# Kernel optimization log

Hardware: AMD Instinct MI355X
Metric: run time of the kernel (lower is better)

Reference implementation:

```python
import jax, jax.numpy as jnp
import numpy as np

N_GRAPHS = 256
EPS = 1e-5


def _bn(x, g, b):
    # training-mode BatchNorm1d: biased batch statistics
    m = jnp.mean(x, axis=0)
    v = jnp.mean((x - m) ** 2, axis=0)
    return (x - m) * jax.lax.rsqrt(v + EPS) * g + b


def _gcn_conv(x, W, b, src, dst, dinv, n_nodes):
    # GCNConv: D^{-1/2} (A + I) D^{-1/2} X W + b
    h = x @ W  # [N, H]
    coef = dinv[src] * dinv[dst]  # [E]
    msg = h[src] * coef[:, None]  # [E, H]
    agg = jax.ops.segment_sum(msg, dst, num_segments=n_nodes)
    agg = agg + h * (dinv * dinv)[:, None]  # self-loop term
    return agg + b


def setup_inputs() -> dict:
    key = jax.random.key(0)
    ks = jax.random.split(key, 20)
    N, E, D, H, C = 50000, 600000, 128, 128, 10
    L = 3  # num_conv_layers
    x = jax.random.normal(ks[0], (N, D), dtype=jnp.float32)
    edge_index = jax.random.randint(ks[1], (2, E), 0, N, dtype=jnp.int64)
    batch = jnp.sort(jax.random.randint(ks[2], (N,), 0, N_GRAPHS, dtype=jnp.int64))

    def xavier(k, shape):
        fan_in, fan_out = shape[0], shape[1]
        lim = float(np.sqrt(6.0 / (fan_in + fan_out)))
        return jax.random.uniform(k, shape, jnp.float32, -lim, lim)

    return {
        "x": x,
        "edge_index": edge_index,
        "batch": batch,
        "bn_feat_g": jnp.ones((D,), jnp.float32),
        "bn_feat_b": jnp.full((D,), 1e-4, jnp.float32),
        "conv_feat_W": xavier(ks[3], (D, H)),
        "conv_feat_b": jnp.zeros((H,), jnp.float32),
        "conv_W": jnp.stack([xavier(ks[4 + i], (H, H)) for i in range(L)]),
        "conv_b": jnp.zeros((L, H), jnp.float32),
        "bn_conv_g": jnp.ones((L, H), jnp.float32),
        "bn_conv_b": jnp.full((L, H), 1e-4, jnp.float32),
        "gate_W1": xavier(ks[8], (H, H)),
        "gate_b1": jnp.zeros((H,), jnp.float32),
        "gate_W2": xavier(ks[9], (H, 1)),
        "gate_b2": jnp.zeros((1,), jnp.float32),
        "fc_W": xavier(ks[10], (H, H)),
        "fc_b": jnp.zeros((H,), jnp.float32),
        "bn_fc_g": jnp.ones((H,), jnp.float32),
        "bn_fc_b": jnp.full((H,), 1e-4, jnp.float32),
        "cls_W": xavier(ks[11], (H, C)),
        "cls_b": jnp.zeros((C,), jnp.float32),
    }


def reference(x, edge_index, batch, bn_feat_g, bn_feat_b, conv_feat_W, conv_feat_b,
              conv_W, conv_b, bn_conv_g, bn_conv_b, gate_W1, gate_b1, gate_W2,
              gate_b2, fc_W, fc_b, bn_fc_g, bn_fc_b, cls_W, cls_b):
    N = x.shape[0]
    src, dst = edge_index[0], edge_index[1]
    # degree incl. self-loop (edge weights = 1)
    deg = jax.ops.segment_sum(jnp.ones_like(src, dtype=x.dtype), dst, num_segments=N) + 1.0
    dinv = jax.lax.rsqrt(deg)

    h = _bn(x, bn_feat_g, bn_feat_b)
    h = jax.nn.relu(_gcn_conv(h, conv_feat_W, conv_feat_b, src, dst, dinv, N))
    for i in range(conv_W.shape[0]):
        h = jax.nn.relu(_gcn_conv(_bn(h, bn_conv_g[i], bn_conv_b[i]),
                                  conv_W[i], conv_b[i], src, dst, dinv, N))
    gate = jax.nn.sigmoid(jax.nn.relu(h @ gate_W1 + gate_b1) @ gate_W2 + gate_b2)  # [N,1]
    g = jax.ops.segment_sum(h * gate, batch, num_segments=N_GRAPHS)  # [G, H]
    g = jax.nn.relu(_bn(g, bn_fc_g, bn_fc_b) @ fc_W + fc_b)
    logits = g @ cls_W + cls_b
    return jax.nn.log_softmax(logits, axis=-1)
```

## Files before the change

kernel.cpp:

```cpp
#include <hip/hip_runtime.h>
#include <hip/hip_fp16.h>

typedef unsigned short u16;
typedef unsigned int u32;
typedef __attribute__((ext_vector_type(8))) short short8;
typedef __attribute__((ext_vector_type(4))) float floatx4;

#define EPSI 1e-5f
#define NCOPY 64

__device__ __forceinline__ float b2f(u16 h) { return __uint_as_float(((u32)h) << 16); }
__device__ __forceinline__ u16 f2b(float f) {
    u32 u = __float_as_uint(f);
    return (u16)((u + 0x7fffu + ((u >> 16) & 1u)) >> 16);
}
__device__ __forceinline__ u32 pack2(float a, float b) {
    return (u32)f2b(a) | ((u32)f2b(b) << 16);
}
__device__ __forceinline__ float ldf(const void* p, int i, int fm) {
    if (fm == 1) return b2f(((const u16*)p)[i]);
    if (fm == 2) return __half2float(__ushort_as_half(((const u16*)p)[i]));
    return ((const float*)p)[i];
}
__device__ __forceinline__ int ldi(const void* p, int i, int im) {
    return im ? ((const int*)p)[2 * i] : ((const int*)p)[i];
}

template <typename T>
__device__ __forceinline__ void ntst(T* p, T v) {
    __builtin_nontemporal_store(v, p);
}

__device__ __forceinline__ void acc8(float* a, int4 v, float w) {
    u32 x = (u32)v.x, y = (u32)v.y, z = (u32)v.z, q = (u32)v.w;
    a[0] += b2f((u16)x) * w;
    a[1] += b2f((u16)(x >> 16)) * w;
    a[2] += b2f((u16)y) * w;
    a[3] += b2f((u16)(y >> 16)) * w;
    a[4] += b2f((u16)z) * w;
    a[5] += b2f((u16)(z >> 16)) * w;
    a[6] += b2f((u16)q) * w;
    a[7] += b2f((u16)(q >> 16)) * w;
}

__global__ void init_kernel(u32* zp, int nz, const void* ones, const void* ei, int* flags) {
    int i = blockIdx.x * 256 + threadIdx.x;
    if (i < nz) zp[i] = 0;
    if (blockIdx.x == 0 && threadIdx.x == 0) {
        u32 w = ((const u32*)ones)[0];
        int fm = 0;
        if (w == 0x3F803F80u) fm = 1;
        else if (w == 0x3C003C00u) fm = 2;
        const u32* e = (const u32*)ei;
        int all0 = 1;
        for (int k = 0; k < 16; ++k)
            if (e[2 * k + 1] != 0u) all0 = 0;
        flags[0] = fm;
        flags[1] = all0;
    }
}

__global__ void bigprep_kernel(const void* __restrict__ ei, int* __restrict__ cnt, int E,
                               const void* __restrict__ batch, int* __restrict__ bounds, int N,
                               int EB, const void* __restrict__ x, u32* __restrict__ A2,
                               float* __restrict__ stats0, const void* __restrict__ gW1,
                               const void* __restrict__ gb1, u16* __restrict__ Wtg,
                               float* __restrict__ bias2g, const void* __restrict__ cfW,
                               const void* __restrict__ cW, u16* __restrict__ Wt4,
                               const void* __restrict__ fcW, float* __restrict__ fcWf,
                               const void* __restrict__ clsW, float* __restrict__ clsWf,
                               const void* __restrict__ fcb, float* __restrict__ fcbf,
                               const void* __restrict__ clsb, float* __restrict__ clsbf,
                               const void* __restrict__ gW2, float* __restrict__ gW2f,
                               const void* __restrict__ gb2, float* __restrict__ gb2f,
                               const void* __restrict__ cfb, const void* __restrict__ cvb,
                               float* __restrict__ biasf, u16* __restrict__ rank,
                               const int* __restrict__ flags) {
    int fm = flags[0];
    int bid = blockIdx.x, t = threadIdx.x;
    if (bid < EB) {
        int im = flags[1];
        int g = bid * 256 + t;
        if (g < E) {
            int r = atomicAdd(&cnt[ldi(ei, E + g, im)], 1);
            rank[g] = (u16)r;
        }
        if (g < N) {
            int b = ldi(batch, g, im);
            if (g == 0) {
                for (int q = 0; q <= b; ++q) bounds[q] = 0;
            } else {
                int bp = ldi(batch, g - 1, im);
                for (int q = bp + 1; q <= b; ++q) bounds[q] = g;
            }
            if (g == N - 1) {
                for (int q = b + 1; q <= 256; ++q) bounds[q] = N;
            }
        }
        return;
    }
    int pid = bid - EB;
    if (pid < 1024) {
        int np = N * 64;
        float s0 = 0.f, s1 = 0.f, q0 = 0.f, q1 = 0.f;
        if (fm == 1) {
            const u32* xs = (const u32*)x;
            for (int j = pid * 256 + t; j < np; j += 1024 * 256) {
                u32 w = xs[j];
                ntst(&A2[j], w);
                float v0 = b2f((u16)w), v1 = b2f((u16)(w >> 16));
                s0 += v0;
                q0 += v0 * v0;
                s1 += v1;
                q1 += v1 * v1;
            }
        } else if (fm == 0) {
            const float2* xs2 = (const float2*)x;
            for (int j = pid * 256 + t; j < np; j += 1024 * 256) {
                float2 v = xs2[j];
                ntst(&A2[j], pack2(v.x, v.y));
                s0 += v.x;
                q0 += v.x * v.x;
                s1 += v.y;
                q1 += v.y * v.y;
            }
        } else {
            for (int j = pid * 256 + t; j < np; j += 1024 * 256) {
                float v0 = ldf(x, 2 * j, fm);
                float v1 = ldf(x, 2 * j + 1, fm);
                ntst(&A2[j], pack2(v0, v1));
                s0 += v0;
                q0 += v0 * v0;
                s1 += v1;
                q1 += v1 * v1;
            }
        }
        __shared__ float2 sh[256];
        sh[t] = make_float2(s0, s1);
        __syncthreads();
        float* so = stats0 + (pid & (NCOPY - 1)) * 256;
        if (t < 64) {
            float a = 0.f, b = 0.f;
#pragma unroll
            for (int w = 0; w < 4; ++w) {
                float2 v = sh[t + w * 64];
                a += v.x;
                b += v.y;
            }
            atomicAdd(&so[2 * t], a);
            atomicAdd(&so[2 * t + 1], b);
        }
        __syncthreads();
        sh[t] = make_float2(q0, q1);
        __syncthreads();
        if (t < 64) {
            float a = 0.f, b = 0.f;
#pragma unroll
            for (int w = 0; w < 4; ++w) {
                float2 v = sh[t + w * 64];
                a += v.x;
                b += v.y;
            }
            atomicAdd(&so[128 + 2 * t], a);
            atomicAdd(&so[128 + 2 * t + 1], b);
        }
    } else if (pid < 1152) {
        int n = pid - 1024;
        if (t < 128) Wtg[n * 128 + t] = f2b(ldf(gW1, t * 128 + n, fm));
        if (t == 0) bias2g[n] = ldf(gb1, n, fm);
    } else if (pid < 1216) {
        int task = pid - 1152;
        int mat = task >> 4, tile = task & 15;
        int tr = (tile >> 2) * 32, tc = (tile & 3) * 32;
        const void* src = mat == 0 ? cfW : cW;
        int soff = mat == 0 ? 0 : (mat - 1) * 16384;
        __shared__ float tb[32][33];
#pragma unroll
        for (int i = 0; i < 4; ++i) {
            int o = t * 4 + i;
            int r = o >> 5, c = o & 31;
            tb[r][c] = ldf(src, soff + (tr + r) * 128 + tc + c, fm);
        }
        __syncthreads();
        u16* dst = Wt4 + mat * 16384;
#pragma unroll
        for (int i = 0; i < 4; ++i) {
            int o = t * 4 + i;
            int nr = o >> 5, kc = o & 31;
            dst[(tc + nr) * 128 + tr + kc] = f2b(tb[kc][nr]);
        }
    } else if (pid < 1224) {
        int base = (pid - 1216) * 2048;
        for (int i = t; i < 2048; i += 256) fcWf[base + i] = ldf(fcW, base + i, fm);
    } else {
        for (int i = t; i < 1280; i += 256) clsWf[i] = ldf(clsW, i, fm);
        for (int i = t; i < 512; i += 256)
            biasf[i] = (i < 128) ? ldf(cfb, i, fm) : ldf(cvb, i - 128, fm);
        if (t < 128) {
            fcbf[t] = ldf(fcb, t, fm);
            gW2f[t] = ldf(gW2, t, fm);
        }
        if (t < 10) clsbf[t] = ldf(clsb, t, fm);
        if (t == 0) gb2f[0] = ldf(gb2, 0, fm);
    }
}

__global__ void scan_kernel(const int* __restrict__ cnt, int* __restrict__ row_start, int n) {
    int b = blockIdx.x, t = threadIdx.x;
    __shared__ int sh[256];
    const int4* c4 = (const int4*)cnt;
    int lim4 = b * 256;
    int acc = 0;
    for (int i = t; i < lim4; i += 256) {
        int4 v = c4[i];
        acc += v.x + v.y + v.z + v.w;
    }
    sh[t] = acc;
    __syncthreads();
    for (int o = 128; o > 0; o >>= 1) {
        if (t < o) sh[t] += sh[t + o];
        __syncthreads();
    }
    int pre = sh[0];
    __syncthreads();
    int base = b * 1024 + t * 4;
    int v[4];
    int s = 0;
#pragma unroll
    for (int j = 0; j < 4; ++j) {
        int idx = base + j;
        v[j] = (idx < n) ? cnt[idx] : 0;
        s += v[j];
    }
    sh[t] = s;
    __syncthreads();
    for (int o = 1; o < 256; o <<= 1) {
        int add = (t >= o) ? sh[t - o] : 0;
        __syncthreads();
        sh[t] += add;
        __syncthreads();
    }
    int run = pre + sh[t] - s;
#pragma unroll
    for (int j = 0; j < 4; ++j) {
        int idx = base + j;
        run += v[j];
        if (idx < n) row_start[idx + 1] = run;
    }
    if (b == 0 && t == 0) row_start[0] = 0;
}

__global__ __launch_bounds__(256) void mfma_fill_kernel(
    const u16* __restrict__ A, const u16* __restrict__ Wt, const float* __restrict__ stats,
    const void* __restrict__ bng, const void* __restrict__ bnb, u16* __restrict__ C, int N,
    int mmgrid, const void* __restrict__ ei, const int* __restrict__ row_start,
    const u16* __restrict__ rank, const int* __restrict__ cnt, u32* __restrict__ edges, int E,
    const int* __restrict__ flags) {
    int t = threadIdx.x;
    if ((int)blockIdx.x >= mmgrid) {
        int im = flags[1];
        int e = (blockIdx.x - mmgrid) * 256 + t;
        if (e < E) {
            int s = ldi(ei, e, im);
            int d = ldi(ei, E + e, im);
            int p = row_start[d] + (int)rank[e];
            float ds = rsqrtf((float)cnt[s] + 1.0f);
            edges[p] = (u32)s | ((u32)__half_as_ushort(__float2half_rn(ds)) << 16);
        }
        return;
    }
    int fm = flags[0];
    __shared__ float scs[128], shs[128];
    if (t < 128) {
        float ms = 0.f, qs = 0.f;
#pragma unroll
        for (int c = 0; c < NCOPY; ++c) {
            ms += stats[c * 256 + t];
            qs += stats[c * 256 + 128 + t];
        }
        float m = ms / (float)N;
        float var = qs / (float)N - m * m;
        float rs = rsqrtf(var + EPSI);
        float sc = rs * ldf(bng, t, fm);
        scs[t] = sc;
        shs[t] = ldf(bnb, t, fm) - m * sc;
    }
    __syncthreads();
    int wid = t >> 6, lane = t & 63;
    int m16 = lane & 15, q = lane >> 4;
    int row0 = blockIdx.x * 64 + wid * 16;
    if (row0 >= N) return;
    int arow = row0 + m16;
    floatx4 acc[8];
#pragma unroll
    for (int i = 0; i < 8; ++i) acc[i] = (floatx4){0.f, 0.f, 0.f, 0.f};
#pragma unroll
    for (int kc = 0; kc < 4; ++kc) {
        short8 af;
        if (arow < N) {
            short8 raw = *(const short8*)&A[(size_t)arow * 128 + kc * 32 + q * 8];
            int k0 = kc * 32 + q * 8;
#pragma unroll
            for (int j = 0; j < 8; ++j)
                af[j] = (short)f2b(b2f((u16)raw[j]) * scs[k0 + j] + shs[k0 + j]);
        } else {
#pragma unroll
            for (int j = 0; j < 8; ++j) af[j] = 0;
        }
#pragma unroll
        for (int nt = 0; nt < 8; ++nt) {
            short8 bf = *(const short8*)&Wt[(nt * 16 + m16) * 128 + kc * 32 + q * 8];
            acc[nt] = __builtin_amdgcn_mfma_f32_16x16x32_bf16(af, bf, acc[nt], 0, 0, 0);
        }
    }
#pragma unroll
    for (int nt = 0; nt < 8; ++nt) {
#pragma unroll
        for (int reg = 0; reg < 4; ++reg) {
            int r = row0 + q * 4 + reg;
            if (r < N) C[(size_t)r * 128 + nt * 16 + m16] = f2b(acc[nt][reg]);
        }
    }
}

__global__ __launch_bounds__(256) void mfma_mm_kernel(
    const u16* __restrict__ A, const u16* __restrict__ Wt, const float* __restrict__ stats,
    const void* __restrict__ bng, const void* __restrict__ bnb, int poff,
    const float* __restrict__ bias2, u16* __restrict__ C, float* __restrict__ gate,
    const float* __restrict__ gW2f, const float* __restrict__ gb2f, int N, int mode,
    const int* __restrict__ flags) {
    int t = threadIdx.x;
    __shared__ float scs[128], shs[128];
    if (stats && t < 128) {
        int fm = flags[0];
        float ms = 0.f, qs = 0.f;
#pragma unroll
        for (int c = 0; c < NCOPY; ++c) {
            ms += stats[c * 256 + t];
            qs += stats[c * 256 + 128 + t];
        }
        float m = ms / (float)N;
        float var = qs / (float)N - m * m;
        float rs = rsqrtf(var + EPSI);
        float sc = rs * ldf(bng, poff + t, fm);
        scs[t] = sc;
        shs[t] = ldf(bnb, poff + t, fm) - m * sc;
    }
    __syncthreads();
    int wid = t >> 6, lane = t & 63;
    int m16 = lane & 15, q = lane >> 4;
    int row0 = blockIdx.x * 64 + wid * 16;
    if (row0 >= N) return;
    int arow = row0 + m16;
    floatx4 acc[8];
#pragma unroll
    for (int i = 0; i < 8; ++i) acc[i] = (floatx4){0.f, 0.f, 0.f, 0.f};
#pragma unroll
    for (int kc = 0; kc < 4; ++kc) {
        short8 af;
        if (arow < N) {
            if (stats) {
                short8 raw = *(const short8*)&A[(size_t)arow * 128 + kc * 32 + q * 8];
                int k0 = kc * 32 + q * 8;
#pragma unroll
                for (int j = 0; j < 8; ++j)
                    af[j] = (short)f2b(b2f((u16)raw[j]) * scs[k0 + j] + shs[k0 + j]);
            } else {
                af = *(const short8*)&A[(size_t)arow * 128 + kc * 32 + q * 8];
            }
        } else {
#pragma unroll
            for (int j = 0; j < 8; ++j) af[j] = 0;
        }
#pragma unroll
        for (int nt = 0; nt < 8; ++nt) {
            short8 bf = *(const short8*)&Wt[(nt * 16 + m16) * 128 + kc * 32 + q * 8];
            acc[nt] = __builtin_amdgcn_mfma_f32_16x16x32_bf16(af, bf, acc[nt], 0, 0, 0);
        }
    }
    if (mode == 0) {
#pragma unroll
        for (int nt = 0; nt < 8; ++nt) {
#pragma unroll
            for (int reg = 0; reg < 4; ++reg) {
                int r = row0 + q * 4 + reg;
                if (r < N) C[(size_t)r * 128 + nt * 16 + m16] = f2b(acc[nt][reg]);
            }
        }
    } else {
        float p[4] = {0.f, 0.f, 0.f, 0.f};
#pragma unroll
        for (int nt = 0; nt < 8; ++nt) {
            float b2v = bias2[nt * 16 + m16];
            float w2v = gW2f[nt * 16 + m16];
#pragma unroll
            for (int reg = 0; reg < 4; ++reg)
                p[reg] += fmaxf(acc[nt][reg] + b2v, 0.0f) * w2v;
        }
        float gb = gb2f[0];
#pragma unroll
        for (int reg = 0; reg < 4; ++reg) {
            float v = p[reg];
            v += __shfl_xor(v, 1);
            v += __shfl_xor(v, 2);
            v += __shfl_xor(v, 4);
            v += __shfl_xor(v, 8);
            if (m16 == 0) {
                int r = row0 + q * 4 + reg;
                if (r < N) gate[r] = 1.0f / (1.0f + expf(-(v + gb)));
            }
        }
    }
}

__global__ __launch_bounds__(512) void agg_kernel(
    const u32* __restrict__ C2, const int* __restrict__ row_start,
    const u32* __restrict__ edges, const float* __restrict__ biasf, int boff,
    u32* __restrict__ A2, float* __restrict__ statsOut, int N) {
    int t = threadIdx.x;
    int wid = t >> 6, lane = t & 63;
    int g = lane >> 4, p = lane & 15;
    __shared__ float xch[8][128];
    __shared__ float2 sh[512];
    float s0 = 0.f, s1 = 0.f, q0 = 0.f, q1 = 0.f;
    int ngrp = (N + 7) / 8;
    for (int gi = blockIdx.x; gi < ngrp; gi += gridDim.x) {
        int n = gi * 8 + wid;
        float acc[8];
#pragma unroll
        for (int j = 0; j < 8; ++j) acc[j] = 0.f;
        float dinv_d = 1.f;
        if (n < N) {
            int rs = row_start[n], re = row_start[n + 1];
            dinv_d = rsqrtf((float)(re - rs) + 1.0f);
            if (g == 0) {
                int4 s = *(const int4*)&C2[(size_t)n * 64 + p * 4];
                acc8(acc, s, dinv_d);
            }
            for (int e = rs; e < re; e += 16) {
                int iA = e + g, iB = e + 4 + g, iC = e + 8 + g, iD = e + 12 + g;
                u32 eA = edges[iA < re ? iA : re - 1];
                u32 eB = edges[iB < re ? iB : re - 1];
                u32 eC = edges[iC < re ? iC : re - 1];
                u32 eD = edges[iD < re ? iD : re - 1];
                int4 vA = *(const int4*)&C2[(size_t)(eA & 0xFFFFu) * 64 + p * 4];
                int4 vB = *(const int4*)&C2[(size_t)(eB & 0xFFFFu) * 64 + p * 4];
                int4 vC = *(const int4*)&C2[(size_t)(eC & 0xFFFFu) * 64 + p * 4];
                int4 vD = *(const int4*)&C2[(size_t)(eD & 0xFFFFu) * 64 + p * 4];
                float wA = iA < re ? __half2float(__ushort_as_half((u16)(eA >> 16))) : 0.f;
                float wB = iB < re ? __half2float(__ushort_as_half((u16)(eB >> 16))) : 0.f;
                float wC = iC < re ? __half2float(__ushort_as_half((u16)(eC >> 16))) : 0.f;
                float wD = iD < re ? __half2float(__ushort_as_half((u16)(eD >> 16))) : 0.f;
                acc8(acc, vA, wA);
                acc8(acc, vB, wB);
                acc8(acc, vC, wC);
                acc8(acc, vD, wD);
            }
        }
#pragma unroll
        for (int j = 0; j < 8; ++j) {
            acc[j] += __shfl_xor(acc[j], 16);
            acc[j] += __shfl_xor(acc[j], 32);
        }
        if (g == 0) {
#pragma unroll
            for (int j = 0; j < 8; ++j) xch[wid][p * 8 + j] = acc[j];
        }
        __syncthreads();
        float ax = 0.f, ay = 0.f;
        if (n < N) {
            float2 bv = ((const float2*)(biasf + boff))[lane];
            float2 v = ((const float2*)xch[wid])[lane];
            ax = fmaxf(v.x * dinv_d + bv.x, 0.0f);
            ay = fmaxf(v.y * dinv_d + bv.y, 0.0f);
            ntst(&A2[(size_t)n * 64 + lane], pack2(ax, ay));
        }
        s0 += ax;
        s1 += ay;
        q0 += ax * ax;
        q1 += ay * ay;
        __syncthreads();
    }
    if (!statsOut) return;
    sh[t] = make_float2(s0, s1);
    __syncthreads();
    float* so = statsOut + (blockIdx.x & (NCOPY - 1)) * 256;
    if (t < 64) {
        float a = 0.f, b = 0.f;
#pragma unroll
        for (int w = 0; w < 8; ++w) {
            float2 v = sh[t + w * 64];
            a += v.x;
            b += v.y;
        }
        atomicAdd(&so[2 * t], a);
        atomicAdd(&so[2 * t + 1], b);
    }
    __syncthreads();
    sh[t] = make_float2(q0, q1);
    __syncthreads();
    if (t < 64) {
        float a = 0.f, b = 0.f;
#pragma unroll
        for (int w = 0; w < 8; ++w) {
            float2 v = sh[t + w * 64];
            a += v.x;
            b += v.y;
        }
        atomicAdd(&so[128 + 2 * t], a);
        atomicAdd(&so[128 + 2 * t + 1], b);
    }
}

__global__ void pool_kernel(const u32* __restrict__ A2, const float* __restrict__ gate,
                            const int* __restrict__ bounds, float* __restrict__ pooled,
                            float* __restrict__ statsP) {
    int g = blockIdx.x;
    int t = threadIdx.x;
    int f2 = t & 63, grp = t >> 6;
    int s = bounds[g], e = bounds[g + 1];
    __shared__ float2 sh[256];
    float ax = 0.f, ay = 0.f;
    int r = s + grp;
    for (; r + 4 < e; r += 8) {
        u32 v0 = A2[(size_t)r * 64 + f2];
        u32 v1 = A2[(size_t)(r + 4) * 64 + f2];
        float g0 = gate[r], g1 = gate[r + 4];
        ax += b2f((u16)v0) * g0;
        ay += b2f((u16)(v0 >> 16)) * g0;
        ax += b2f((u16)v1) * g1;
        ay += b2f((u16)(v1 >> 16)) * g1;
    }
    if (r < e) {
        u32 v0 = A2[(size_t)r * 64 + f2];
        float g0 = gate[r];
        ax += b2f((u16)v0) * g0;
        ay += b2f((u16)(v0 >> 16)) * g0;
    }
    sh[t] = make_float2(ax, ay);
    __syncthreads();
    if (t < 64) {
        float2 a = sh[t], b = sh[t + 64], c = sh[t + 128], d = sh[t + 192];
        float x = a.x + b.x + c.x + d.x;
        float y = a.y + b.y + c.y + d.y;
        ((float2*)(pooled + g * 128))[t] = make_float2(x, y);
        float* so = statsP + (g & 7) * 256;
        atomicAdd(&so[2 * t], x);
        atomicAdd(&so[2 * t + 1], y);
        atomicAdd(&so[128 + 2 * t], x * x);
        atomicAdd(&so[128 + 2 * t + 1], y * y);
    }
}

__global__ __launch_bounds__(256) void fc_cls_kernel(
    const float* __restrict__ pooled, const float* __restrict__ statsP,
    const void* __restrict__ bng, const void* __restrict__ bnb,
    const float* __restrict__ fcWf, const float* __restrict__ fcbf,
    const float* __restrict__ clsWf, const float* __restrict__ clsbf, void* __restrict__ out,
    const int* __restrict__ flags) {
    int fm = flags[0];
    int g = blockIdx.x, t = threadIdx.x;
    __shared__ float pv[128];
    __shared__ float red[256];
    __shared__ float fco[128];
    __shared__ float lg[10];
    __shared__ float redv[2];
    if (t < 128) {
        float ms = 0.f, qs = 0.f;
#pragma unroll
        for (int c = 0; c < 8; ++c) {
            ms += statsP[c * 256 + t];
            qs += statsP[c * 256 + 128 + t];
        }
        float m = ms / 256.0f;
        float var = qs / 256.0f - m * m;
        float rs = rsqrtf(var + EPSI);
        float sc = rs * ldf(bng, t, fm);
        pv[t] = pooled[g * 128 + t] * sc + (ldf(bnb, t, fm) - m * sc);
    }
    __syncthreads();
    {
        int j = t & 127, half = t >> 7;
        float acc = 0.f;
        int k0 = half * 64;
#pragma unroll 8
        for (int k = k0; k < k0 + 64; ++k) acc += pv[k] * fcWf[k * 128 + j];
        red[t] = acc;
    }
    __syncthreads();
    if (t < 128) fco[t] = fmaxf(red[t] + red[t + 128] + fcbf[t], 0.0f);
    __syncthreads();
    if (t < 10) {
        float a = clsbf[t];
#pragma unroll 8
        for (int k = 0; k < 128; ++k) a += fco[k] * clsWf[k * 10 + t];
        lg[t] = a;
    }
    __syncthreads();
    if (t == 0) {
        float mx = lg[0];
        for (int j = 1; j < 10; ++j) mx = fmaxf(mx, lg[j]);
        float se = 0.f;
        for (int j = 0; j < 10; ++j) se += expf(lg[j] - mx);
        redv[0] = mx;
        redv[1] = logf(se);
    }
    __syncthreads();
    if (t < 10) {
        float v = lg[t] - redv[0] - redv[1];
        if (fm == 1) ((u16*)out)[g * 10 + t] = f2b(v);
        else if (fm == 2) ((u16*)out)[g * 10 + t] = __half_as_ushort(__float2half(v));
        else ((float*)out)[g * 10 + t] = v;
    }
}

extern "C" void kernel_launch(void* const* d_in, const int* in_sizes, int n_in,
                              void* d_out, int out_size, void* d_ws, size_t ws_size,
                              hipStream_t stream) {
    const void* x = d_in[0];
    const void* ei = d_in[1];
    const void* batch = d_in[2];
    const void* bn_feat_g = d_in[3];
    const void* bn_feat_b = d_in[4];
    const void* conv_feat_W = d_in[5];
    const void* conv_feat_b = d_in[6];
    const void* conv_W = d_in[7];
    const void* conv_b = d_in[8];
    const void* bn_conv_g = d_in[9];
    const void* bn_conv_b = d_in[10];
    const void* gate_W1 = d_in[11];
    const void* gate_b1 = d_in[12];
    const void* gate_W2 = d_in[13];
    const void* gate_b2 = d_in[14];
    const void* fc_W = d_in[15];
    const void* fc_b = d_in[16];
    const void* bn_fc_g = d_in[17];
    const void* bn_fc_b = d_in[18];
    const void* cls_W = d_in[19];
    const void* cls_b = d_in[20];

    const int N = in_sizes[2];
    const int E = in_sizes[1] / 2;
    const int NB = (N + 1023) / 1024;
    const int EB = ((E > N ? E : N) + 255) / 256;

    u32* ws = (u32*)d_ws;
    size_t off = 0;
    auto alloc = [&](size_t n) {
        size_t o = off;
        off += (n + 63) & ~(size_t)63;
        return o;
    };
    size_t o_cnt = alloc(N);
    size_t o_stats = alloc(5 * NCOPY * 256);
    size_t o_statsP = alloc(2048);
    size_t zero_end = off;
    size_t o_flags = alloc(16);
    size_t o_rs = alloc((size_t)N + 1);
    size_t o_edges = alloc((size_t)E);
    size_t o_rank = alloc(((size_t)E + 1) / 2);
    size_t o_wtg = alloc(128 * 128 / 2);
    size_t o_b2g = alloc(128);
    size_t o_Wt4 = alloc(4 * 16384 / 2);
    size_t o_fcW = alloc(16384);
    size_t o_fcb = alloc(128);
    size_t o_clsW = alloc(1280);
    size_t o_clsb = alloc(16);
    size_t o_gW2 = alloc(128);
    size_t o_gb2 = alloc(16);
    size_t o_biasf = alloc(512);
    size_t o_gate = alloc(N);
    size_t o_bnd = alloc(257);
    size_t o_pool = alloc(256 * 128);
    size_t o_A = alloc((size_t)N * 64);
    size_t o_C = alloc((size_t)N * 64);
    (void)ws_size;
    (void)n_in;
    (void)out_size;

    int* cnt = (int*)(ws + o_cnt);
    float* stats = (float*)(ws + o_stats);
    float* statsP = (float*)(ws + o_statsP);
    int* flags = (int*)(ws + o_flags);
    int* row_start = (int*)(ws + o_rs);
    u32* edges = (u32*)(ws + o_edges);
    u16* rank = (u16*)(ws + o_rank);
    u16* Wtg = (u16*)(ws + o_wtg);
    float* bias2g = (float*)(ws + o_b2g);
    u16* Wt4 = (u16*)(ws + o_Wt4);
    float* fcWf = (float*)(ws + o_fcW);
    float* fcbf = (float*)(ws + o_fcb);
    float* clsWf = (float*)(ws + o_clsW);
    float* clsbf = (float*)(ws + o_clsb);
    float* gW2f = (float*)(ws + o_gW2);
    float* gb2f = (float*)(ws + o_gb2);
    float* biasf = (float*)(ws + o_biasf);
    float* gateb = (float*)(ws + o_gate);
    int* bnd = (int*)(ws + o_bnd);
    float* pooled = (float*)(ws + o_pool);
    u16* A = (u16*)(ws + o_A);
    u16* C = (u16*)(ws + o_C);

    int nz = (int)zero_end;
    init_kernel<<<(nz + 255) / 256, 256, 0, stream>>>(ws, nz, bn_feat_g, ei, flags);
    bigprep_kernel<<<EB + 1225, 256, 0, stream>>>(
        ei, cnt, E, batch, bnd, N, EB, x, (u32*)A, stats, gate_W1, gate_b1, Wtg, bias2g,
        conv_feat_W, conv_W, Wt4, fc_W, fcWf, cls_W, clsWf, fc_b, fcbf, cls_b, clsbf, gate_W2,
        gW2f, gate_b2, gb2f, conv_feat_b, conv_b, biasf, rank, flags);
    scan_kernel<<<NB, 256, 0, stream>>>(cnt, row_start, N);

    int mmgrid = (N + 63) / 64;
    int ngrp = (N + 7) / 8;
    int agggrid = ngrp < 2560 ? ngrp : 2560;
    mfma_fill_kernel<<<mmgrid + EB, 256, 0, stream>>>(A, Wt4, stats, bn_feat_g, bn_feat_b, C, N,
                                                      mmgrid, ei, row_start, rank, cnt, edges,
                                                      E, flags);
    for (int l = 0; l < 4; ++l) {
        if (l > 0)
            mfma_mm_kernel<<<mmgrid, 256, 0, stream>>>(
                A, Wt4 + (size_t)l * 16384, stats + (size_t)l * (NCOPY * 256), bn_conv_g,
                bn_conv_b, (l - 1) * 128, nullptr, C, nullptr, nullptr, nullptr, N, 0, flags);
        float* so = (l < 3) ? stats + (size_t)(l + 1) * (NCOPY * 256) : nullptr;
        agg_kernel<<<agggrid, 512, 0, stream>>>((const u32*)C, row_start, edges, biasf, l * 128,
                                                (u32*)A, so, N);
    }

    mfma_mm_kernel<<<mmgrid, 256, 0, stream>>>(A, Wtg, nullptr, nullptr, nullptr, 0, bias2g,
                                               nullptr, gateb, gW2f, gb2f, N, 2, flags);
    pool_kernel<<<256, 256, 0, stream>>>((const u32*)A, gateb, bnd, pooled, statsP);
    fc_cls_kernel<<<256, 256, 0, stream>>>(pooled, statsP, bn_fc_g, bn_fc_b, fcWf, fcbf, clsWf,
                                           clsbf, d_out, flags);
}
```

Before: 440.0 us.

## Fuse GCN aggregation, BatchNorm and weight matmul into one per-layer kernel

Reorders each GCN layer to aggregate first (A·h) and then apply the BatchNorm affine transform and the weight matmul via MFMA inside one kernel. The BN shift is folded in using the per-node weighted degree sum. ReLU, bias and next-layer statistics are produced in the same pass, ping-ponging between two buffers. This removes a separate matmul kernel and one intermediate round trip to global memory per layer, and splits edge filling into its own kernel. In exchange, each fused block now does extra syncthreads and smaller MFMA tiles per group of 16 nodes.

```diff
diff --git a/kernel.cpp b/kernel.cpp
--- a/kernel.cpp
+++ b/kernel.cpp
@@ -250,42 +250,151 @@
     if (b == 0 && t == 0) row_start[0] = 0;
 }
 
-__global__ __launch_bounds__(256) void mfma_fill_kernel(
-    const u16* __restrict__ A, const u16* __restrict__ Wt, const float* __restrict__ stats,
-    const void* __restrict__ bng, const void* __restrict__ bnb, u16* __restrict__ C, int N,
-    int mmgrid, const void* __restrict__ ei, const int* __restrict__ row_start,
-    const u16* __restrict__ rank, const int* __restrict__ cnt, u32* __restrict__ edges, int E,
-    const int* __restrict__ flags) {
+__global__ void fill_kernel(const void* __restrict__ ei, const int* __restrict__ row_start,
+                            const u16* __restrict__ rank, const int* __restrict__ cnt,
+                            u32* __restrict__ edges, int E, const int* __restrict__ flags) {
+    int im = flags[1];
+    int e = blockIdx.x * 256 + threadIdx.x;
+    if (e < E) {
+        int s = ldi(ei, e, im);
+        int d = ldi(ei, E + e, im);
+        int p = row_start[d] + (int)rank[e];
+        float ds = rsqrtf((float)cnt[s] + 1.0f);
+        edges[p] = (u32)s | ((u32)__half_as_ushort(__float2half_rn(ds)) << 16);
+    }
+}
+
+__global__ __launch_bounds__(512) void fused_kernel(
+    const u32* __restrict__ hin, u32* __restrict__ hout, const int* __restrict__ row_start,
+    const u32* __restrict__ edges, const float* __restrict__ stats_in,
+    const void* __restrict__ bng, const void* __restrict__ bnb, int poff,
+    const u16* __restrict__ Wt, const float* __restrict__ biasf, int boff,
+    float* __restrict__ statsOut, int N, const int* __restrict__ flags) {
     int t = threadIdx.x;
-    if ((int)blockIdx.x >= mmgrid) {
-        int im = flags[1];
-        int e = (blockIdx.x - mmgrid) * 256 + t;
-        if (e < E) {
-            int s = ldi(ei, e, im);
-            int d = ldi(ei, E + e, im);
-            int p = row_start[d] + (int)rank[e];
-            float ds = rsqrtf((float)cnt[s] + 1.0f);
-            edges[p] = (u32)s | ((u32)__half_as_ushort(__float2half_rn(ds)) << 16);
-        }
-        return;
-    }
+    int wid = t >> 6, lane = t & 63;
+    int g = lane >> 4, p = lane & 15;
+    int m16 = lane & 15, q = lane >> 4;
     int fm = flags[0];
     __shared__ float scs[128], shs[128];
+    __shared__ float xch[8][128];
+    __shared__ u32 zbuf[16][64];
+    __shared__ float sred[128], sred2[128];
     if (t < 128) {
         float ms = 0.f, qs = 0.f;
 #pragma unroll
         for (int c = 0; c < NCOPY; ++c) {
-            ms += stats[c * 256 + t];
-            qs += stats[c * 256 + 128 + t];
+            ms += stats_in[c * 256 + t];
+            qs += stats_in[c * 256 + 128 + t];
         }
         float m = ms / (float)N;
         float var = qs / (float)N - m * m;
         float rs = rsqrtf(var + EPSI);
-        float sc = rs * ldf(bng, t, fm);
+        float sc = rs * ldf(bng, poff + t, fm);
         scs[t] = sc;
-        shs[t] = ldf(bnb, t, fm) - m * sc;
-    }
-    __syncthreads();
+        shs[t] = ldf(bnb, poff + t, fm) - m * sc;
+        sred[t] = 0.f;
+        sred2[t] = 0.f;
+    }
+    __syncthreads();
+    float ss = 0.f, sq = 0.f;
+    int ngrp = (N + 15) / 16;
+    for (int gi = blockIdx.x; gi < ngrp; gi += gridDim.x) {
+        int base = gi * 16;
+        for (int half = 0; half < 2; ++half) {
+            int lr = half * 8 + wid;
+            int n = base + lr;
+            float acc[8];
+#pragma unroll
+            for (int j = 0; j < 8; ++j) acc[j] = 0.f;
+            float wsum = 0.f, dinv = 1.f;
+            if (n < N) {
+                int rs = row_start[n], re = row_start[n + 1];
+                dinv = rsqrtf((float)(re - rs) + 1.0f);
+                if (g == 0) {
+                    int4 s = *(const int4*)&hin[(size_t)n * 64 + p * 4];
+                    acc8(acc, s, dinv);
+                }
+                for (int e = rs; e < re; e += 16) {
+                    int iA = e + g, iB = e + 4 + g, iC = e + 8 + g, iD = e + 12 + g;
+                    u32 eA = edges[iA < re ? iA : re - 1];
+                    u32 eB = edges[iB < re ? iB : re - 1];
+                    u32 eC = edges[iC < re ? iC : re - 1];
+                    u32 eD = edges[iD < re ? iD : re - 1];
+                    int4 vA = *(const int4*)&hin[(size_t)(eA & 0xFFFFu) * 64 + p * 4];
+                    int4 vB = *(const int4*)&hin[(size_t)(eB & 0xFFFFu) * 64 + p * 4];
+                    int4 vC = *(const int4*)&hin[(size_t)(eC & 0xFFFFu) * 64 + p * 4];
+                    int4 vD = *(const int4*)&hin[(size_t)(eD & 0xFFFFu) * 64 + p * 4];
+                    float wA = iA < re ? __half2float(__ushort_as_half((u16)(eA >> 16))) : 0.f;
+                    float wB = iB < re ? __half2float(__ushort_as_half((u16)(eB >> 16))) : 0.f;
+                    float wC = iC < re ? __half2float(__ushort_as_half((u16)(eC >> 16))) : 0.f;
+                    float wD = iD < re ? __half2float(__ushort_as_half((u16)(eD >> 16))) : 0.f;
+                    acc8(acc, vA, wA);
+                    acc8(acc, vB, wB);
+                    acc8(acc, vC, wC);
+                    acc8(acc, vD, wD);
+                    wsum += wA + wB + wC + wD;
+                }
+            }
+#pragma unroll
+            for (int j = 0; j < 8; ++j) {
+                acc[j] += __shfl_xor(acc[j], 16);
+                acc[j] += __shfl_xor(acc[j], 32);
+            }
+            wsum += __shfl_xor(wsum, 16);
+            wsum += __shfl_xor(wsum, 32);
+            if (g == 0) {
+#pragma unroll
+                for (int j = 0; j < 8; ++j) xch[wid][p * 8 + j] = acc[j];
+            }
+            __syncthreads();
+            {
+                float2 v = ((const float2*)xch[wid])[lane];
+                float Wz = dinv * (wsum + dinv);
+                float zx = scs[2 * lane] * (v.x * dinv) + Wz * shs[2 * lane];
+                float zy = scs[2 * lane + 1] * (v.y * dinv) + Wz * shs[2 * lane + 1];
+                zbuf[lr][lane] = pack2(zx, zy);
+            }
+            __syncthreads();
+        }
+        floatx4 acc4 = (floatx4){0.f, 0.f, 0.f, 0.f};
+        const u16* zb = (const u16*)zbuf;
+#pragma unroll
+        for (int kc = 0; kc < 4; ++kc) {
+            short8 af = *(const short8*)&zb[m16 * 128 + kc * 32 + q * 8];
+            short8 bf = *(const short8*)&Wt[(wid * 16 + m16) * 128 + kc * 32 + q * 8];
+            acc4 = __builtin_amdgcn_mfma_f32_16x16x32_bf16(af, bf, acc4, 0, 0, 0);
+        }
+        int c = wid * 16 + m16;
+        float bv = biasf[boff + c];
+#pragma unroll
+        for (int reg = 0; reg < 4; ++reg) {
+            int n2 = base + q * 4 + reg;
+            if (n2 < N) {
+                float val = fmaxf(acc4[reg] + bv, 0.0f);
+                ((u16*)hout)[(size_t)n2 * 128 + c] = f2b(val);
+                ss += val;
+                sq += val * val;
+            }
+        }
+        __syncthreads();
+    }
+    if (!statsOut) return;
+    int c = wid * 16 + m16;
+    atomicAdd(&sred[c], ss);
+    atomicAdd(&sred2[c], sq);
+    __syncthreads();
+    if (t < 128) {
+        float* so = statsOut + (blockIdx.x & (NCOPY - 1)) * 256;
+        atomicAdd(&so[t], sred[t]);
+        atomicAdd(&so[128 + t], sred2[t]);
+    }
+}
+
+__global__ __launch_bounds__(256) void mfma_mm_kernel(
+    const u16* __restrict__ A, const u16* __restrict__ Wt, const float* __restrict__ bias2,
+    float* __restrict__ gate, const float* __restrict__ gW2f, const float* __restrict__ gb2f,
+    int N) {
+    int t = threadIdx.x;
     int wid = t >> 6, lane = t & 63;
     int m16 = lane & 15, q = lane >> 4;
     int row0 = blockIdx.x * 64 + wid * 16;
@@ -298,11 +407,7 @@
     for (int kc = 0; kc < 4; ++kc) {
         short8 af;
         if (arow < N) {
-            short8 raw = *(const short8*)&A[(size_t)arow * 128 + kc * 32 + q * 8];
-            int k0 = kc * 32 + q * 8;
-#pragma unroll
-            for (int j = 0; j < 8; ++j)
-                af[j] = (short)f2b(b2f((u16)raw[j]) * scs[k0 + j] + shs[k0 + j]);
+            af = *(const short8*)&A[(size_t)arow * 128 + kc * 32 + q * 8];
         } else {
 #pragma unroll
             for (int j = 0; j < 8; ++j) af[j] = 0;
@@ -313,202 +418,26 @@
             acc[nt] = __builtin_amdgcn_mfma_f32_16x16x32_bf16(af, bf, acc[nt], 0, 0, 0);
         }
     }
+    float pp[4] = {0.f, 0.f, 0.f, 0.f};
 #pragma unroll
     for (int nt = 0; nt < 8; ++nt) {
-#pragma unroll
-        for (int reg = 0; reg < 4; ++reg) {
+        float b2v = bias2[nt * 16 + m16];
+        float w2v = gW2f[nt * 16 + m16];
+#pragma unroll
+        for (int reg = 0; reg < 4; ++reg) pp[reg] += fmaxf(acc[nt][reg] + b2v, 0.0f) * w2v;
+    }
+    float gb = gb2f[0];
+#pragma unroll
+    for (int reg = 0; reg < 4; ++reg) {
+        float v = pp[reg];
+        v += __shfl_xor(v, 1);
+        v += __shfl_xor(v, 2);
+        v += __shfl_xor(v, 4);
+        v += __shfl_xor(v, 8);
+        if (m16 == 0) {
             int r = row0 + q * 4 + reg;
-            if (r < N) C[(size_t)r * 128 + nt * 16 + m16] = f2b(acc[nt][reg]);
-        }
-    }
-}
-
-__global__ __launch_bounds__(256) void mfma_mm_kernel(
-    const u16* __restrict__ A, const u16* __restrict__ Wt, const float* __restrict__ stats,
-    const void* __restrict__ bng, const void* __restrict__ bnb, int poff,
-    const float* __restrict__ bias2, u16* __restrict__ C, float* __restrict__ gate,
-    const float* __restrict__ gW2f, const float* __restrict__ gb2f, int N, int mode,
-    const int* __restrict__ flags) {
-    int t = threadIdx.x;
-    __shared__ float scs[128], shs[128];
-    if (stats && t < 128) {
-        int fm = flags[0];
-        float ms = 0.f, qs = 0.f;
-#pragma unroll
-        for (int c = 0; c < NCOPY; ++c) {
-            ms += stats[c * 256 + t];
-            qs += stats[c * 256 + 128 + t];
-        }
-        float m = ms / (float)N;
-        float var = qs / (float)N - m * m;
-        float rs = rsqrtf(var + EPSI);
-        float sc = rs * ldf(bng, poff + t, fm);
-        scs[t] = sc;
-        shs[t] = ldf(bnb, poff + t, fm) - m * sc;
-    }
-    __syncthreads();
-    int wid = t >> 6, lane = t & 63;
-    int m16 = lane & 15, q = lane >> 4;
-    int row0 = blockIdx.x * 64 + wid * 16;
-    if (row0 >= N) return;
-    int arow = row0 + m16;
-    floatx4 acc[8];
-#pragma unroll
-    for (int i = 0; i < 8; ++i) acc[i] = (floatx4){0.f, 0.f, 0.f, 0.f};
-#pragma unroll
-    for (int kc = 0; kc < 4; ++kc) {
-        short8 af;
-        if (arow < N) {
-            if (stats) {
-                short8 raw = *(const short8*)&A[(size_t)arow * 128 + kc * 32 + q * 8];
-                int k0 = kc * 32 + q * 8;
-#pragma unroll
-                for (int j = 0; j < 8; ++j)
-                    af[j] = (short)f2b(b2f((u16)raw[j]) * scs[k0 + j] + shs[k0 + j]);
-            } else {
-                af = *(const short8*)&A[(size_t)arow * 128 + kc * 32 + q * 8];
-            }
-        } else {
-#pragma unroll
-            for (int j = 0; j < 8; ++j) af[j] = 0;
-        }
-#pragma unroll
-        for (int nt = 0; nt < 8; ++nt) {
-            short8 bf = *(const short8*)&Wt[(nt * 16 + m16) * 128 + kc * 32 + q * 8];
-            acc[nt] = __builtin_amdgcn_mfma_f32_16x16x32_bf16(af, bf, acc[nt], 0, 0, 0);
-        }
-    }
-    if (mode == 0) {
-#pragma unroll
-        for (int nt = 0; nt < 8; ++nt) {
-#pragma unroll
-            for (int reg = 0; reg < 4; ++reg) {
-                int r = row0 + q * 4 + reg;
-                if (r < N) C[(size_t)r * 128 + nt * 16 + m16] = f2b(acc[nt][reg]);
-            }
-        }
-    } else {
-        float p[4] = {0.f, 0.f, 0.f, 0.f};
-#pragma unroll
-        for (int nt = 0; nt < 8; ++nt) {
-            float b2v = bias2[nt * 16 + m16];
-            float w2v = gW2f[nt * 16 + m16];
-#pragma unroll
-            for (int reg = 0; reg < 4; ++reg)
-                p[reg] += fmaxf(acc[nt][reg] + b2v, 0.0f) * w2v;
-        }
-        float gb = gb2f[0];
-#pragma unroll
-        for (int reg = 0; reg < 4; ++reg) {
-            float v = p[reg];
-            v += __shfl_xor(v, 1);
-            v += __shfl_xor(v, 2);
-            v += __shfl_xor(v, 4);
-            v += __shfl_xor(v, 8);
-            if (m16 == 0) {
-                int r = row0 + q * 4 + reg;
-                if (r < N) gate[r] = 1.0f / (1.0f + expf(-(v + gb)));
-            }
-        }
-    }
-}
-
-__global__ __launch_bounds__(512) void agg_kernel(
-    const u32* __restrict__ C2, const int* __restrict__ row_start,
-    const u32* __restrict__ edges, const float* __restrict__ biasf, int boff,
-    u32* __restrict__ A2, float* __restrict__ statsOut, int N) {
-    int t = threadIdx.x;
-    int wid = t >> 6, lane = t & 63;
-    int g = lane >> 4, p = lane & 15;
-    __shared__ float xch[8][128];
-    __shared__ float2 sh[512];
-    float s0 = 0.f, s1 = 0.f, q0 = 0.f, q1 = 0.f;
-    int ngrp = (N + 7) / 8;
-    for (int gi = blockIdx.x; gi < ngrp; gi += gridDim.x) {
-        int n = gi * 8 + wid;
-        float acc[8];
-#pragma unroll
-        for (int j = 0; j < 8; ++j) acc[j] = 0.f;
-        float dinv_d = 1.f;
-        if (n < N) {
-            int rs = row_start[n], re = row_start[n + 1];
-            dinv_d = rsqrtf((float)(re - rs) + 1.0f);
-            if (g == 0) {
-                int4 s = *(const int4*)&C2[(size_t)n * 64 + p * 4];
-                acc8(acc, s, dinv_d);
-            }
-            for (int e = rs; e < re; e += 16) {
-                int iA = e + g, iB = e + 4 + g, iC = e + 8 + g, iD = e + 12 + g;
-                u32 eA = edges[iA < re ? iA : re - 1];
-                u32 eB = edges[iB < re ? iB : re - 1];
-                u32 eC = edges[iC < re ? iC : re - 1];
-                u32 eD = edges[iD < re ? iD : re - 1];
-                int4 vA = *(const int4*)&C2[(size_t)(eA & 0xFFFFu) * 64 + p * 4];
-                int4 vB = *(const int4*)&C2[(size_t)(eB & 0xFFFFu) * 64 + p * 4];
-                int4 vC = *(const int4*)&C2[(size_t)(eC & 0xFFFFu) * 64 + p * 4];
-                int4 vD = *(const int4*)&C2[(size_t)(eD & 0xFFFFu) * 64 + p * 4];
-                float wA = iA < re ? __half2float(__ushort_as_half((u16)(eA >> 16))) : 0.f;
-                float wB = iB < re ? __half2float(__ushort_as_half((u16)(eB >> 16))) : 0.f;
-                float wC = iC < re ? __half2float(__ushort_as_half((u16)(eC >> 16))) : 0.f;
-                float wD = iD < re ? __half2float(__ushort_as_half((u16)(eD >> 16))) : 0.f;
-                acc8(acc, vA, wA);
-                acc8(acc, vB, wB);
-                acc8(acc, vC, wC);
-                acc8(acc, vD, wD);
-            }
-        }
-#pragma unroll
-        for (int j = 0; j < 8; ++j) {
-            acc[j] += __shfl_xor(acc[j], 16);
-            acc[j] += __shfl_xor(acc[j], 32);
-        }
-        if (g == 0) {
-#pragma unroll
-            for (int j = 0; j < 8; ++j) xch[wid][p * 8 + j] = acc[j];
-        }
-        __syncthreads();
-        float ax = 0.f, ay = 0.f;
-        if (n < N) {
-            float2 bv = ((const float2*)(biasf + boff))[lane];
-            float2 v = ((const float2*)xch[wid])[lane];
-            ax = fmaxf(v.x * dinv_d + bv.x, 0.0f);
-            ay = fmaxf(v.y * dinv_d + bv.y, 0.0f);
-            ntst(&A2[(size_t)n * 64 + lane], pack2(ax, ay));
-        }
-        s0 += ax;
-        s1 += ay;
-        q0 += ax * ax;
-        q1 += ay * ay;
-        __syncthreads();
-    }
-    if (!statsOut) return;
-    sh[t] = make_float2(s0, s1);
-    __syncthreads();
-    float* so = statsOut + (blockIdx.x & (NCOPY - 1)) * 256;
-    if (t < 64) {
-        float a = 0.f, b = 0.f;
-#pragma unroll
-        for (int w = 0; w < 8; ++w) {
-            float2 v = sh[t + w * 64];
-            a += v.x;
-            b += v.y;
-        }
-        atomicAdd(&so[2 * t], a);
-        atomicAdd(&so[2 * t + 1], b);
-    }
-    __syncthreads();
-    sh[t] = make_float2(q0, q1);
-    __syncthreads();
-    if (t < 64) {
-        float a = 0.f, b = 0.f;
-#pragma unroll
-        for (int w = 0; w < 8; ++w) {
-            float2 v = sh[t + w * 64];
-            a += v.x;
-            b += v.y;
-        }
-        atomicAdd(&so[128 + 2 * t], a);
-        atomicAdd(&so[128 + 2 * t + 1], b);
+            if (r < N) gate[r] = 1.0f / (1.0f + expf(-(v + gb)));
+        }
     }
 }
 
@@ -708,25 +637,24 @@
         conv_feat_W, conv_W, Wt4, fc_W, fcWf, cls_W, clsWf, fc_b, fcbf, cls_b, clsbf, gate_W2,
         gW2f, gate_b2, gb2f, conv_feat_b, conv_b, biasf, rank, flags);
     scan_kernel<<<NB, 256, 0, stream>>>(cnt, row_start, N);
+    fill_kernel<<<EB, 256, 0, stream>>>(ei, row_start, rank, cnt, edges, E, flags);
+
+    int ngrp16 = (N + 15) / 16;
+    int fgrid = ngrp16 < 2560 ? ngrp16 : 2560;
+    u32* hbuf[2] = {(u32*)A, (u32*)C};
+    for (int l = 0; l < 4; ++l) {
+        const void* bg = (l == 0) ? bn_feat_g : bn_conv_g;
+        const void* bb = (l == 0) ? bn_feat_b : bn_conv_b;
+        int poff = (l == 0) ? 0 : (l - 1) * 128;
+        float* so = (l < 3) ? stats + (size_t)(l + 1) * (NCOPY * 256) : nullptr;
+        fused_kernel<<<fgrid, 512, 0, stream>>>(
+            hbuf[l & 1], hbuf[(l + 1) & 1], row_start, edges,
+            stats + (size_t)l * (NCOPY * 256), bg, bb, poff, Wt4 + (size_t)l * 16384, biasf,
+            l * 128, so, N, flags);
+    }
 
     int mmgrid = (N + 63) / 64;
-    int ngrp = (N + 7) / 8;
-    int agggrid = ngrp < 2560 ? ngrp : 2560;
-    mfma_fill_kernel<<<mmgrid + EB, 256, 0, stream>>>(A, Wt4, stats, bn_feat_g, bn_feat_b, C, N,
-                                                      mmgrid, ei, row_start, rank, cnt, edges,
-                                                      E, flags);
-    for (int l = 0; l < 4; ++l) {
-        if (l > 0)
-            mfma_mm_kernel<<<mmgrid, 256, 0, stream>>>(
-                A, Wt4 + (size_t)l * 16384, stats + (size_t)l * (NCOPY * 256), bn_conv_g,
-                bn_conv_b, (l - 1) * 128, nullptr, C, nullptr, nullptr, nullptr, N, 0, flags);
-        float* so = (l < 3) ? stats + (size_t)(l + 1) * (NCOPY * 256) : nullptr;
-        agg_kernel<<<agggrid, 512, 0, stream>>>((const u32*)C, row_start, edges, biasf, l * 128,
-                                                (u32*)A, so, N);
-    }
-
-    mfma_mm_kernel<<<mmgrid, 256, 0, stream>>>(A, Wtg, nullptr, nullptr, nullptr, 0, bias2g,
-                                               nullptr, gateb, gW2f, gb2f, N, 2, flags);
+    mfma_mm_kernel<<<mmgrid, 256, 0, stream>>>(A, Wtg, bias2g, gateb, gW2f, gb2f, N);
     pool_kernel<<<256, 256, 0, stream>>>((const u32*)A, gateb, bnd, pooled, statsP);
     fc_cls_kernel<<<256, 256, 0, stream>>>(pooled, statsP, bn_fc_g, bn_fc_b, fcWf, fcbf, clsWf,
                                            clsbf, d_out, flags);
```

Result: slower. 602.4 us (+36.9%).
